# Kernel optimization log

Measured on AMD Instinct MI355X. Metric: run time of the kernel, lower is better.

## Reference

```python
import jax, jax.numpy as jnp
import numpy as np

B, S, E, H = 8, 2048, 1024, 64

def setup_inputs() -> dict:
    key = jax.random.key(0)
    ks = jax.random.split(key, 10)
    inp = {
        'input_Q': jax.random.normal(ks[0], (B, S, E), dtype=jnp.float32),
        'input_K': jax.random.normal(ks[1], (B, S, E), dtype=jnp.float32),
        'input_V': jax.random.normal(ks[2], (B, S, E), dtype=jnp.float32),
        'mask': jax.random.randint(ks[3], (B, S, S), 0, 2) > 0,
        # Linear params: torch Linear(E, H) -> weight [H, E], use as x @ W^T + b; store transposed [E, H]
        'Wq': jax.random.normal(ks[4], (E, H), dtype=jnp.float32) / np.sqrt(E),
        'bq': jnp.zeros((H,), dtype=jnp.float32),
        'Wk': jax.random.normal(ks[5], (E, H), dtype=jnp.float32) / np.sqrt(E),
        'bk': jnp.zeros((H,), dtype=jnp.float32),
        'Wv': jax.random.normal(ks[6], (E, H), dtype=jnp.float32) / np.sqrt(E),
        'bv': jnp.zeros((H,), dtype=jnp.float32),
    }
    return inp

def reference(input_Q, input_K, input_V, mask, Wq, bq, Wk, bk, Wv, bv):
    Q = jnp.einsum('bse,eh->bsh', input_Q, Wq) + bq  # [B,S,H]
    K = jnp.einsum('bse,eh->bsh', input_K, Wk) + bk
    V = jnp.einsum('bse,eh->bsh', input_V, Wv) + bv
    scores = jnp.einsum('bqh,bkh->bqk', Q, K) / np.sqrt(H).astype(np.float32)  # [B,S,S]
    # faithful to masked_fill_(mask, 1e-10) BEFORE softmax
    scores = jnp.where(mask, jnp.float32(1e-10), scores)
    attn = jax.nn.softmax(scores, axis=-1)
    # dropout is identity in eval/reference mode
    return jnp.einsum('bqk,bkh->bqh', attn, V)
```

## Files before the change

kernel.cpp:

```cpp
#include <hip/hip_runtime.h>
#include <hip/hip_bf16.h>
#include <stdint.h>

constexpr int Bc = 8, Sc = 2048, Ec = 1024, Hc = 64;

typedef __bf16 bf16x8 __attribute__((ext_vector_type(8)));
typedef float f32x4 __attribute__((ext_vector_type(4)));
typedef unsigned short ushort8 __attribute__((ext_vector_type(8)));
typedef unsigned short ushort4v __attribute__((ext_vector_type(4)));

static __device__ __forceinline__ unsigned short f2bf(float f) {
  uint32_t u = __builtin_bit_cast(uint32_t, f);
  u = u + 0x7fffu + ((u >> 16) & 1u);
  return (unsigned short)(u >> 16);
}
static __device__ __forceinline__ bf16x8 ldb8(const unsigned short* p) {
  return __builtin_bit_cast(bf16x8, *(const ushort8*)p);
}
static __device__ __forceinline__ uint32_t pk2bf(float a, float b) {
  return (uint32_t)f2bf(a) | ((uint32_t)f2bf(b) << 16);
}

__global__ __launch_bounds__(256) void wt_kernel(
    const float* __restrict__ Wq, const float* __restrict__ Wk,
    const float* __restrict__ Wv, unsigned short* __restrict__ Wt) {
  int idx = blockIdx.x * 256 + threadIdx.x;
  int m = idx >> 16;
  int r = idx & 65535;
  int h = r >> 10;
  int e = r & 1023;
  const float* W = (m == 0) ? Wq : (m == 1) ? Wk : Wv;
  float scale = (m == 0) ? 0.125f : 1.0f;
  Wt[idx] = f2bf(W[e * Hc + h] * scale);
}

__global__ __launch_bounds__(256, 4) void proj_kernel(
    const float* __restrict__ Xq, const float* __restrict__ Xk,
    const float* __restrict__ Xv, const float* __restrict__ bq,
    const float* __restrict__ bk, const float* __restrict__ bv,
    const unsigned short* __restrict__ Wt,
    unsigned short* __restrict__ Qb, unsigned short* __restrict__ Kb,
    unsigned short* __restrict__ Vt) {
  const int mat = blockIdx.y;
  const float* X = (mat == 0) ? Xq : (mat == 1) ? Xk : Xv;
  const float* bias = (mat == 0) ? bq : (mat == 1) ? bk : bv;
  const float bscale = (mat == 0) ? 0.125f : 1.0f;
  const unsigned short* W = Wt + mat * (Hc * Ec);

  const int tid = threadIdx.x;
  const int wave = tid >> 6, lane = tid & 63;
  const int row0 = blockIdx.x * 64;

  __shared__ unsigned short As[64][72];
  __shared__ unsigned short Ws[64][72];

  const int xrow = tid >> 4;
  const int xcol = (tid & 15) * 4;
  const float* xptr = X + (size_t)(row0 + xrow) * Ec + xcol;

  float4 xr[4];
  ushort8 wr[2];

  auto load_chunk = [&](int c) {
    const int k0 = c * 64;
#pragma unroll
    for (int p = 0; p < 4; p++)
      xr[p] = *(const float4*)(xptr + (size_t)(p * 16) * Ec + k0);
#pragma unroll
    for (int i = 0; i < 2; i++) {
      int j = i * 256 + tid;
      int h = j >> 3, kg = j & 7;
      wr[i] = *(const ushort8*)(W + (size_t)h * Ec + k0 + kg * 8);
    }
  };

  f32x4 acc[4];
#pragma unroll
  for (int nt = 0; nt < 4; nt++) acc[nt] = (f32x4){0.f, 0.f, 0.f, 0.f};

  load_chunk(0);

  for (int c = 0; c < 16; c++) {
#pragma unroll
    for (int p = 0; p < 4; p++) {
      ushort4v v = __builtin_bit_cast(
          ushort4v, (uint2){pk2bf(xr[p].x, xr[p].y), pk2bf(xr[p].z, xr[p].w)});
      *(ushort4v*)&As[p * 16 + xrow][xcol] = v;
    }
#pragma unroll
    for (int i = 0; i < 2; i++) {
      int j = i * 256 + tid;
      *(ushort8*)&Ws[j >> 3][(j & 7) * 8] = wr[i];
    }
    __syncthreads();

    if (c < 15) load_chunk(c + 1);

#pragma unroll
    for (int kk = 0; kk < 2; kk++) {
      bf16x8 aA = ldb8(&As[wave * 16 + (lane & 15)][kk * 32 + (lane >> 4) * 8]);
#pragma unroll
      for (int nt = 0; nt < 4; nt++) {
        bf16x8 bW = ldb8(&Ws[nt * 16 + (lane & 15)][kk * 32 + (lane >> 4) * 8]);
        acc[nt] = __builtin_amdgcn_mfma_f32_16x16x32_bf16(aA, bW, acc[nt], 0, 0, 0);
      }
    }
    __syncthreads();
  }

#pragma unroll
  for (int nt = 0; nt < 4; nt++) {
    float bcol = bias[nt * 16 + (lane & 15)] * bscale;
#pragma unroll
    for (int r = 0; r < 4; r++)
      As[wave * 16 + (lane >> 4) * 4 + r][nt * 16 + (lane & 15)] =
          f2bf(acc[nt][r] + bcol);
  }
  __syncthreads();

  if (mat < 2) {
    unsigned short* out = (mat == 0) ? Qb : Kb;
    int s_l = tid >> 2;
    int hs = (tid & 3) * 16;
    ushort8 v0 = *(const ushort8*)&As[s_l][hs];
    ushort8 v1 = *(const ushort8*)&As[s_l][hs + 8];
    unsigned short* dst = out + (size_t)(row0 + s_l) * Hc + hs;
    *(ushort8*)dst = v0;
    *(ushort8*)(dst + 8) = v1;
  } else {
    int h = tid >> 2;
    int ss = (tid & 3) * 16;
    int bb = row0 >> 11;
    int sbase = (row0 & 2047) + ss;
    ushort8 v0, v1;
#pragma unroll
    for (int i = 0; i < 8; i++) {
      v0[i] = As[ss + i][h];
      v1[i] = As[ss + 8 + i][h];
    }
    unsigned short* dst = Vt + ((size_t)bb * Hc + h) * Sc + sbase;
    *(ushort8*)dst = v0;
    *(ushort8*)(dst + 8) = v1;
  }
}

__global__ __launch_bounds__(256, 4) void attn_kernel(
    const unsigned short* __restrict__ Qb, const unsigned short* __restrict__ Kb,
    const unsigned short* __restrict__ Vt, const int* __restrict__ mask,
    float* __restrict__ out) {
  const int id = blockIdx.x;
  const int b = id & 7;
  const int q0 = (id >> 3) * 16;
  const int tid = threadIdx.x;
  const int wave = tid >> 6, lane = tid & 63;

  __shared__ unsigned short Ps[4][16][72];
  __shared__ float sm[4][16], sl[4][16];
  __shared__ float Os[4][16][64];

  const unsigned short* qptr =
      Qb + ((size_t)b * Sc + q0 + (lane & 15)) * Hc + (lane >> 4) * 8;
  bf16x8 aQ0 = ldb8(qptr);
  bf16x8 aQ1 = ldb8(qptr + 32);

  float m_r[4], l_r[4];
  f32x4 Oacc[4];
#pragma unroll
  for (int r = 0; r < 4; r++) { m_r[r] = -INFINITY; l_r[r] = 0.f; }
#pragma unroll
  for (int ht = 0; ht < 4; ht++) Oacc[ht] = (f32x4){0.f, 0.f, 0.f, 0.f};

  const int* mrow[4];
#pragma unroll
  for (int r = 0; r < 4; r++)
    mrow[r] = mask + ((size_t)b * Sc + q0 + (lane >> 4) * 4 + r) * Sc + (lane & 15);

  const unsigned short* kbase =
      Kb + ((size_t)b * Sc) * Hc + (size_t)(lane & 15) * Hc + (lane >> 4) * 8;
  const unsigned short* vbase[4];
#pragma unroll
  for (int ht = 0; ht < 4; ht++)
    vbase[ht] = Vt + ((size_t)b * Hc + ht * 16 + (lane & 15)) * Sc + (lane >> 4) * 8;

  const int kw = wave * 512;
  int mva[4][4], mvb[4][4];

  auto issue_mask = [&](int koff, int (&mv)[4][4]) {
#pragma unroll
    for (int nt = 0; nt < 4; nt++)
#pragma unroll
      for (int r = 0; r < 4; r++) mv[nt][r] = mrow[r][koff + nt * 16];
  };
  auto compress = [&](const int (&mv)[4][4]) -> uint32_t {
    uint32_t bits = 0;
#pragma unroll
    for (int nt = 0; nt < 4; nt++)
#pragma unroll
      for (int r = 0; r < 4; r++)
        bits |= (mv[nt][r] ? 1u : 0u) << (nt * 4 + r);
    return bits;
  };

  auto process = [&](int koff, uint32_t bits) {
    float sv[4][4];
#pragma unroll
    for (int nt = 0; nt < 4; nt++) {
      const unsigned short* kp = kbase + (size_t)(koff + nt * 16) * Hc;
      bf16x8 bK0 = ldb8(kp);
      bf16x8 bK1 = ldb8(kp + 32);
      f32x4 s = (f32x4){0.f, 0.f, 0.f, 0.f};
      s = __builtin_amdgcn_mfma_f32_16x16x32_bf16(aQ0, bK0, s, 0, 0, 0);
      s = __builtin_amdgcn_mfma_f32_16x16x32_bf16(aQ1, bK1, s, 0, 0, 0);
#pragma unroll
      for (int r = 0; r < 4; r++)
        sv[nt][r] = ((bits >> (nt * 4 + r)) & 1u) ? 1e-10f : s[r];
    }

    float rmax[4];
#pragma unroll
    for (int r = 0; r < 4; r++) {
      rmax[r] = fmaxf(fmaxf(sv[0][r], sv[1][r]), fmaxf(sv[2][r], sv[3][r]));
#pragma unroll
      for (int off = 1; off < 16; off <<= 1)
        rmax[r] = fmaxf(rmax[r], __shfl_xor(rmax[r], off, 64));
    }

    float alpha[4], p[4][4], psum[4];
#pragma unroll
    for (int r = 0; r < 4; r++) {
      float mnew = fmaxf(m_r[r], rmax[r]);
      alpha[r] = __expf(m_r[r] - mnew);
      m_r[r] = mnew;
      psum[r] = 0.f;
    }
#pragma unroll
    for (int nt = 0; nt < 4; nt++)
#pragma unroll
      for (int r = 0; r < 4; r++) {
        p[nt][r] = __expf(sv[nt][r] - m_r[r]);
        psum[r] += p[nt][r];
      }
#pragma unroll
    for (int r = 0; r < 4; r++) {
#pragma unroll
      for (int off = 1; off < 16; off <<= 1)
        psum[r] += __shfl_xor(psum[r], off, 64);
      l_r[r] = l_r[r] * alpha[r] + psum[r];
    }
#pragma unroll
    for (int ht = 0; ht < 4; ht++)
#pragma unroll
      for (int r = 0; r < 4; r++) Oacc[ht][r] *= alpha[r];

#pragma unroll
    for (int nt = 0; nt < 4; nt++)
#pragma unroll
      for (int r = 0; r < 4; r++)
        Ps[wave][(lane >> 4) * 4 + r][nt * 16 + (lane & 15)] = f2bf(p[nt][r]);

#pragma unroll
    for (int ks = 0; ks < 2; ks++) {
      bf16x8 aP = ldb8(&Ps[wave][lane & 15][ks * 32 + (lane >> 4) * 8]);
#pragma unroll
      for (int ht = 0; ht < 4; ht++) {
        bf16x8 bV = ldb8(vbase[ht] + koff + ks * 32);
        Oacc[ht] = __builtin_amdgcn_mfma_f32_16x16x32_bf16(aP, bV, Oacc[ht], 0, 0, 0);
      }
    }
  };

  issue_mask(kw, mva);
  for (int c2 = 0; c2 < 8; c2 += 2) {
    issue_mask(kw + (c2 + 1) * 64, mvb);
    process(kw + c2 * 64, compress(mva));
    if (c2 + 2 < 8) issue_mask(kw + (c2 + 2) * 64, mva);
    process(kw + (c2 + 1) * 64, compress(mvb));
  }

  if ((lane & 15) == 0) {
#pragma unroll
    for (int r = 0; r < 4; r++) {
      sm[wave][(lane >> 4) * 4 + r] = m_r[r];
      sl[wave][(lane >> 4) * 4 + r] = l_r[r];
    }
  }
  __syncthreads();

  float coef[4];
#pragma unroll
  for (int r = 0; r < 4; r++) {
    int row = (lane >> 4) * 4 + r;
    float M = fmaxf(fmaxf(sm[0][row], sm[1][row]), fmaxf(sm[2][row], sm[3][row]));
    coef[r] = __expf(m_r[r] - M);
  }
#pragma unroll
  for (int ht = 0; ht < 4; ht++)
#pragma unroll
    for (int r = 0; r < 4; r++)
      Os[wave][(lane >> 4) * 4 + r][ht * 16 + (lane & 15)] = Oacc[ht][r] * coef[r];
  __syncthreads();

  {
#pragma unroll
    for (int i = 0; i < 4; i++) {
      int row = wave * 4 + i;
      float M = fmaxf(fmaxf(sm[0][row], sm[1][row]), fmaxf(sm[2][row], sm[3][row]));
      float L = sl[0][row] * __expf(sm[0][row] - M) +
                sl[1][row] * __expf(sm[1][row] - M) +
                sl[2][row] * __expf(sm[2][row] - M) +
                sl[3][row] * __expf(sm[3][row] - M);
      float acc = Os[0][row][lane] + Os[1][row][lane] +
                  Os[2][row][lane] + Os[3][row][lane];
      out[((size_t)b * Sc + q0 + row) * Hc + lane] = acc / L;
    }
  }
}

extern "C" void kernel_launch(void* const* d_in, const int* in_sizes, int n_in,
                              void* d_out, int out_size, void* d_ws, size_t ws_size,
                              hipStream_t stream) {
  const float* Xq = (const float*)d_in[0];
  const float* Xk = (const float*)d_in[1];
  const float* Xv = (const float*)d_in[2];
  const int* mask = (const int*)d_in[3];
  const float* Wq = (const float*)d_in[4];
  const float* bq = (const float*)d_in[5];
  const float* Wk = (const float*)d_in[6];
  const float* bk = (const float*)d_in[7];
  const float* Wv = (const float*)d_in[8];
  const float* bv = (const float*)d_in[9];

  unsigned short* Qb = (unsigned short*)d_ws;
  unsigned short* Kb = Qb + (size_t)Bc * Sc * Hc;
  unsigned short* Vt = Kb + (size_t)Bc * Sc * Hc;
  unsigned short* Wt = Vt + (size_t)Bc * Sc * Hc;

  wt_kernel<<<dim3(3 * Hc * Ec / 256), 256, 0, stream>>>(Wq, Wk, Wv, Wt);
  proj_kernel<<<dim3(Bc * Sc / 64, 3), 256, 0, stream>>>(Xq, Xk, Xv, bq, bk, bv,
                                                         Wt, Qb, Kb, Vt);
  attn_kernel<<<dim3(Bc * Sc / 16), 256, 0, stream>>>(Qb, Kb, Vt, mask,
                                                      (float*)d_out);
}
```

Measured before the change: 399.4 us.

## Load projection operands directly into MFMA registers, bypassing shared memory

The projection kernel no longer stages X and W tiles through shared memory. Each lane now loads its MFMA fragment straight from global memory (X as fp32, converted to bf16 in registers, and W as bf16) with a two-stage register double buffer over 32-wide k chunks. This removes the LDS writes, LDS reads and the per-chunk barriers. In exchange each wave re-reads the full W tile from global/L2 and the global access patterns are less coalesced, since each lane reads 32-byte strided segments.

```diff
diff --git a/kernel.cpp b/kernel.cpp
--- a/kernel.cpp
+++ b/kernel.cpp
@@ -8,6 +8,7 @@
 typedef float f32x4 __attribute__((ext_vector_type(4)));
 typedef unsigned short ushort8 __attribute__((ext_vector_type(8)));
 typedef unsigned short ushort4v __attribute__((ext_vector_type(4)));
+typedef uint32_t uint32x4 __attribute__((ext_vector_type(4)));
 
 static __device__ __forceinline__ unsigned short f2bf(float f) {
   uint32_t u = __builtin_bit_cast(uint32_t, f);
@@ -49,72 +50,76 @@
 
   const int tid = threadIdx.x;
   const int wave = tid >> 6, lane = tid & 63;
+  const int rl = lane & 15, kg = lane >> 4;
   const int row0 = blockIdx.x * 64;
 
   __shared__ unsigned short As[64][72];
-  __shared__ unsigned short Ws[64][72];
-
-  const int xrow = tid >> 4;
-  const int xcol = (tid & 15) * 4;
-  const float* xptr = X + (size_t)(row0 + xrow) * Ec + xcol;
-
-  float4 xr[4];
-  ushort8 wr[2];
-
-  auto load_chunk = [&](int c) {
-    const int k0 = c * 64;
-#pragma unroll
-    for (int p = 0; p < 4; p++)
-      xr[p] = *(const float4*)(xptr + (size_t)(p * 16) * Ec + k0);
-#pragma unroll
-    for (int i = 0; i < 2; i++) {
-      int j = i * 256 + tid;
-      int h = j >> 3, kg = j & 7;
-      wr[i] = *(const ushort8*)(W + (size_t)h * Ec + k0 + kg * 8);
-    }
-  };
+
+  const float* xp = X + (size_t)(row0 + wave * 16 + rl) * Ec + kg * 8;
+  const unsigned short* wp0 = W + (size_t)(0 * 16 + rl) * Ec + kg * 8;
+  const unsigned short* wp1 = W + (size_t)(1 * 16 + rl) * Ec + kg * 8;
+  const unsigned short* wp2 = W + (size_t)(2 * 16 + rl) * Ec + kg * 8;
+  const unsigned short* wp3 = W + (size_t)(3 * 16 + rl) * Ec + kg * 8;
 
   f32x4 acc[4];
 #pragma unroll
   for (int nt = 0; nt < 4; nt++) acc[nt] = (f32x4){0.f, 0.f, 0.f, 0.f};
 
-  load_chunk(0);
-
-  for (int c = 0; c < 16; c++) {
-#pragma unroll
-    for (int p = 0; p < 4; p++) {
-      ushort4v v = __builtin_bit_cast(
-          ushort4v, (uint2){pk2bf(xr[p].x, xr[p].y), pk2bf(xr[p].z, xr[p].w)});
-      *(ushort4v*)&As[p * 16 + xrow][xcol] = v;
-    }
-#pragma unroll
-    for (int i = 0; i < 2; i++) {
-      int j = i * 256 + tid;
-      *(ushort8*)&Ws[j >> 3][(j & 7) * 8] = wr[i];
-    }
-    __syncthreads();
-
-    if (c < 15) load_chunk(c + 1);
-
-#pragma unroll
-    for (int kk = 0; kk < 2; kk++) {
-      bf16x8 aA = ldb8(&As[wave * 16 + (lane & 15)][kk * 32 + (lane >> 4) * 8]);
-#pragma unroll
-      for (int nt = 0; nt < 4; nt++) {
-        bf16x8 bW = ldb8(&Ws[nt * 16 + (lane & 15)][kk * 32 + (lane >> 4) * 8]);
-        acc[nt] = __builtin_amdgcn_mfma_f32_16x16x32_bf16(aA, bW, acc[nt], 0, 0, 0);
-      }
-    }
-    __syncthreads();
-  }
+  float4 xa0, xa1, xb0, xb1;
+  ushort8 wa0, wa1, wa2, wa3, wb0, wb1, wb2, wb3;
+
+#define LOAD_A(c)                                    \
+  do {                                               \
+    const float* p_ = xp + (c) * 32;                 \
+    xa0 = *(const float4*)p_;                        \
+    xa1 = *(const float4*)(p_ + 4);                  \
+    wa0 = *(const ushort8*)(wp0 + (c) * 32);         \
+    wa1 = *(const ushort8*)(wp1 + (c) * 32);         \
+    wa2 = *(const ushort8*)(wp2 + (c) * 32);         \
+    wa3 = *(const ushort8*)(wp3 + (c) * 32);         \
+  } while (0)
+#define LOAD_B(c)                                    \
+  do {                                               \
+    const float* p_ = xp + (c) * 32;                 \
+    xb0 = *(const float4*)p_;                        \
+    xb1 = *(const float4*)(p_ + 4);                  \
+    wb0 = *(const ushort8*)(wp0 + (c) * 32);         \
+    wb1 = *(const ushort8*)(wp1 + (c) * 32);         \
+    wb2 = *(const ushort8*)(wp2 + (c) * 32);         \
+    wb3 = *(const ushort8*)(wp3 + (c) * 32);         \
+  } while (0)
+#define PROC(x0, x1, w0, w1, w2, w3)                                      \
+  do {                                                                    \
+    uint32x4 u_ = (uint32x4){pk2bf((x0).x, (x0).y), pk2bf((x0).z, (x0).w),\
+                             pk2bf((x1).x, (x1).y), pk2bf((x1).z, (x1).w)};\
+    bf16x8 aX_ = __builtin_bit_cast(bf16x8, u_);                          \
+    acc[0] = __builtin_amdgcn_mfma_f32_16x16x32_bf16(                     \
+        aX_, __builtin_bit_cast(bf16x8, w0), acc[0], 0, 0, 0);            \
+    acc[1] = __builtin_amdgcn_mfma_f32_16x16x32_bf16(                     \
+        aX_, __builtin_bit_cast(bf16x8, w1), acc[1], 0, 0, 0);            \
+    acc[2] = __builtin_amdgcn_mfma_f32_16x16x32_bf16(                     \
+        aX_, __builtin_bit_cast(bf16x8, w2), acc[2], 0, 0, 0);            \
+    acc[3] = __builtin_amdgcn_mfma_f32_16x16x32_bf16(                     \
+        aX_, __builtin_bit_cast(bf16x8, w3), acc[3], 0, 0, 0);            \
+  } while (0)
+
+  LOAD_A(0);
+  for (int c = 0; c < 32; c += 2) {
+    LOAD_B(c + 1);
+    PROC(xa0, xa1, wa0, wa1, wa2, wa3);
+    if (c + 2 < 32) LOAD_A(c + 2);
+    PROC(xb0, xb1, wb0, wb1, wb2, wb3);
+  }
+#undef LOAD_A
+#undef LOAD_B
+#undef PROC
 
 #pragma unroll
   for (int nt = 0; nt < 4; nt++) {
-    float bcol = bias[nt * 16 + (lane & 15)] * bscale;
+    float bcol = bias[nt * 16 + rl] * bscale;
 #pragma unroll
     for (int r = 0; r < 4; r++)
-      As[wave * 16 + (lane >> 4) * 4 + r][nt * 16 + (lane & 15)] =
-          f2bf(acc[nt][r] + bcol);
+      As[wave * 16 + kg * 4 + r][nt * 16 + rl] = f2bf(acc[nt][r] + bcol);
   }
   __syncthreads();
 
```

Result: no change. 404.4 us (+1.3%).

## Split projection K dimension across waves and drop LDS staging

Applied to the files above, without the earlier changes.

The projection kernel now handles 16 rows per block instead of 64, and each of the 4 waves owns a quarter of the 1024-wide reduction. Each lane loads X and the transposed weights straight from global memory into MFMA operands, with no shared-memory tiles and no per-chunk barriers. Partial sums are reduced through a small fp32 shared slab, then the bias is added and Q/K or transposed V is written out. The grid is four times larger to expose more parallelism for the bandwidth-bound fp32 input read, at the cost of more weight reloads from cache and an extra cross-wave reduction.

```diff
diff --git a/kernel.cpp b/kernel.cpp
--- a/kernel.cpp
+++ b/kernel.cpp
@@ -8,6 +8,7 @@
 typedef float f32x4 __attribute__((ext_vector_type(4)));
 typedef unsigned short ushort8 __attribute__((ext_vector_type(8)));
 typedef unsigned short ushort4v __attribute__((ext_vector_type(4)));
+typedef uint32_t uint32x4 __attribute__((ext_vector_type(4)));
 
 static __device__ __forceinline__ unsigned short f2bf(float f) {
   uint32_t u = __builtin_bit_cast(uint32_t, f);
@@ -34,7 +35,7 @@
   Wt[idx] = f2bf(W[e * Hc + h] * scale);
 }
 
-__global__ __launch_bounds__(256, 4) void proj_kernel(
+__global__ __launch_bounds__(256, 8) void proj_kernel(
     const float* __restrict__ Xq, const float* __restrict__ Xk,
     const float* __restrict__ Xv, const float* __restrict__ bq,
     const float* __restrict__ bk, const float* __restrict__ bv,
@@ -49,98 +50,79 @@
 
   const int tid = threadIdx.x;
   const int wave = tid >> 6, lane = tid & 63;
-  const int row0 = blockIdx.x * 64;
-
-  __shared__ unsigned short As[64][72];
-  __shared__ unsigned short Ws[64][72];
-
-  const int xrow = tid >> 4;
-  const int xcol = (tid & 15) * 4;
-  const float* xptr = X + (size_t)(row0 + xrow) * Ec + xcol;
-
-  float4 xr[4];
-  ushort8 wr[2];
-
-  auto load_chunk = [&](int c) {
-    const int k0 = c * 64;
-#pragma unroll
-    for (int p = 0; p < 4; p++)
-      xr[p] = *(const float4*)(xptr + (size_t)(p * 16) * Ec + k0);
-#pragma unroll
-    for (int i = 0; i < 2; i++) {
-      int j = i * 256 + tid;
-      int h = j >> 3, kg = j & 7;
-      wr[i] = *(const ushort8*)(W + (size_t)h * Ec + k0 + kg * 8);
-    }
-  };
+  const int rl = lane & 15, kg = lane >> 4;
+  const int row0 = blockIdx.x * 16;
+  const int kw = wave * 256;
+
+  __shared__ float slab[4][16][64];
+
+  const float* xp = X + (size_t)(row0 + rl) * Ec + kw + kg * 8;
+  const unsigned short* wp0 = W + (size_t)(0 * 16 + rl) * Ec + kw + kg * 8;
+  const unsigned short* wp1 = W + (size_t)(1 * 16 + rl) * Ec + kw + kg * 8;
+  const unsigned short* wp2 = W + (size_t)(2 * 16 + rl) * Ec + kw + kg * 8;
+  const unsigned short* wp3 = W + (size_t)(3 * 16 + rl) * Ec + kw + kg * 8;
 
   f32x4 acc[4];
 #pragma unroll
   for (int nt = 0; nt < 4; nt++) acc[nt] = (f32x4){0.f, 0.f, 0.f, 0.f};
 
-  load_chunk(0);
-
-  for (int c = 0; c < 16; c++) {
-#pragma unroll
-    for (int p = 0; p < 4; p++) {
-      ushort4v v = __builtin_bit_cast(
-          ushort4v, (uint2){pk2bf(xr[p].x, xr[p].y), pk2bf(xr[p].z, xr[p].w)});
-      *(ushort4v*)&As[p * 16 + xrow][xcol] = v;
-    }
-#pragma unroll
-    for (int i = 0; i < 2; i++) {
-      int j = i * 256 + tid;
-      *(ushort8*)&Ws[j >> 3][(j & 7) * 8] = wr[i];
-    }
-    __syncthreads();
-
-    if (c < 15) load_chunk(c + 1);
-
-#pragma unroll
-    for (int kk = 0; kk < 2; kk++) {
-      bf16x8 aA = ldb8(&As[wave * 16 + (lane & 15)][kk * 32 + (lane >> 4) * 8]);
-#pragma unroll
-      for (int nt = 0; nt < 4; nt++) {
-        bf16x8 bW = ldb8(&Ws[nt * 16 + (lane & 15)][kk * 32 + (lane >> 4) * 8]);
-        acc[nt] = __builtin_amdgcn_mfma_f32_16x16x32_bf16(aA, bW, acc[nt], 0, 0, 0);
-      }
-    }
-    __syncthreads();
-  }
-
-#pragma unroll
-  for (int nt = 0; nt < 4; nt++) {
-    float bcol = bias[nt * 16 + (lane & 15)] * bscale;
+#pragma unroll
+  for (int c = 0; c < 8; c++) {
+    float4 x0 = *(const float4*)(xp + c * 32);
+    float4 x1 = *(const float4*)(xp + c * 32 + 4);
+    ushort8 w0 = *(const ushort8*)(wp0 + c * 32);
+    ushort8 w1 = *(const ushort8*)(wp1 + c * 32);
+    ushort8 w2 = *(const ushort8*)(wp2 + c * 32);
+    ushort8 w3 = *(const ushort8*)(wp3 + c * 32);
+    uint32x4 u = (uint32x4){pk2bf(x0.x, x0.y), pk2bf(x0.z, x0.w),
+                            pk2bf(x1.x, x1.y), pk2bf(x1.z, x1.w)};
+    bf16x8 aX = __builtin_bit_cast(bf16x8, u);
+    acc[0] = __builtin_amdgcn_mfma_f32_16x16x32_bf16(
+        aX, __builtin_bit_cast(bf16x8, w0), acc[0], 0, 0, 0);
+    acc[1] = __builtin_amdgcn_mfma_f32_16x16x32_bf16(
+        aX, __builtin_bit_cast(bf16x8, w1), acc[1], 0, 0, 0);
+    acc[2] = __builtin_amdgcn_mfma_f32_16x16x32_bf16(
+        aX, __builtin_bit_cast(bf16x8, w2), acc[2], 0, 0, 0);
+    acc[3] = __builtin_amdgcn_mfma_f32_16x16x32_bf16(
+        aX, __builtin_bit_cast(bf16x8, w3), acc[3], 0, 0, 0);
+  }
+
+#pragma unroll
+  for (int nt = 0; nt < 4; nt++)
 #pragma unroll
     for (int r = 0; r < 4; r++)
-      As[wave * 16 + (lane >> 4) * 4 + r][nt * 16 + (lane & 15)] =
-          f2bf(acc[nt][r] + bcol);
-  }
+      slab[wave][kg * 4 + r][nt * 16 + rl] = acc[nt][r];
   __syncthreads();
 
   if (mat < 2) {
     unsigned short* out = (mat == 0) ? Qb : Kb;
-    int s_l = tid >> 2;
-    int hs = (tid & 3) * 16;
-    ushort8 v0 = *(const ushort8*)&As[s_l][hs];
-    ushort8 v1 = *(const ushort8*)&As[s_l][hs + 8];
-    unsigned short* dst = out + (size_t)(row0 + s_l) * Hc + hs;
-    *(ushort8*)dst = v0;
-    *(ushort8*)(dst + 8) = v1;
+    int row = wave * 4 + (lane >> 4);
+    int col0 = (lane & 15) * 4;
+    f32x4 s0 = *(const f32x4*)&slab[0][row][col0];
+    f32x4 s1 = *(const f32x4*)&slab[1][row][col0];
+    f32x4 s2 = *(const f32x4*)&slab[2][row][col0];
+    f32x4 s3 = *(const f32x4*)&slab[3][row][col0];
+    float4 bv4 = *(const float4*)(bias + col0);
+    f32x4 v = s0 + s1 + s2 + s3;
+    v[0] += bv4.x * bscale; v[1] += bv4.y * bscale;
+    v[2] += bv4.z * bscale; v[3] += bv4.w * bscale;
+    ushort4v o;
+#pragma unroll
+    for (int i = 0; i < 4; i++) o[i] = f2bf(v[i]);
+    *(ushort4v*)(out + (size_t)(row0 + row) * Hc + col0) = o;
   } else {
-    int h = tid >> 2;
-    int ss = (tid & 3) * 16;
+    int h = lane;
     int bb = row0 >> 11;
-    int sbase = (row0 & 2047) + ss;
-    ushort8 v0, v1;
-#pragma unroll
-    for (int i = 0; i < 8; i++) {
-      v0[i] = As[ss + i][h];
-      v1[i] = As[ss + 8 + i][h];
-    }
-    unsigned short* dst = Vt + ((size_t)bb * Hc + h) * Sc + sbase;
-    *(ushort8*)dst = v0;
-    *(ushort8*)(dst + 8) = v1;
+    int sbase = (row0 & 2047) + wave * 4;
+    float bh = bias[h];
+    ushort4v o;
+#pragma unroll
+    for (int r = 0; r < 4; r++) {
+      float v = slab[0][wave * 4 + r][h] + slab[1][wave * 4 + r][h] +
+                slab[2][wave * 4 + r][h] + slab[3][wave * 4 + r][h] + bh;
+      o[r] = f2bf(v);
+    }
+    *(ushort4v*)(Vt + ((size_t)bb * Hc + h) * Sc + sbase) = o;
   }
 }
 
@@ -336,7 +318,7 @@
   unsigned short* Wt = Vt + (size_t)Bc * Sc * Hc;
 
   wt_kernel<<<dim3(3 * Hc * Ec / 256), 256, 0, stream>>>(Wq, Wk, Wv, Wt);
-  proj_kernel<<<dim3(Bc * Sc / 64, 3), 256, 0, stream>>>(Xq, Xk, Xv, bq, bk, bv,
+  proj_kernel<<<dim3(Bc * Sc / 16, 3), 256, 0, stream>>>(Xq, Xk, Xv, bq, bk, bv,
                                                          Wt, Qb, Kb, Vt);
   attn_kernel<<<dim3(Bc * Sc / 16), 256, 0, stream>>>(Qb, Kb, Vt, mask,
                                                       (float*)d_out);
```

New measurement: 410.1 us. 1.03x slower.
